# Kernel optimization log

Measured on AMD Instinct MI355X. Metric: run time of the kernel, lower is better.

The kernel has to match this reference:

```python
import jax, jax.numpy as jnp
import numpy as np
from jax import lax

B, C_IN, C_OUT, H, W, K, PAD = 4, 64, 64, 96, 96, 3, 1
K2 = K * K


def setup_inputs() -> dict:
    key = jax.random.key(0)
    k1, k2, k3, k4, k5 = jax.random.split(key, 5)
    x = jax.random.normal(k1, (B, C_IN, H, W), jnp.float32)
    offset = jax.random.normal(k2, (B, 2 * K2, H, W), jnp.float32)
    weight = jax.random.normal(k3, (C_OUT, C_IN, K, K), jnp.float32) * 0.05
    mask_weight = jax.random.normal(k4, (K2, C_IN, K, K), jnp.float32) * 0.05
    mask_bias = jax.random.normal(k5, (K2,), jnp.float32) * 0.05
    return {"x": x, "offset": offset, "weight": weight,
            "mask_weight": mask_weight, "mask_bias": mask_bias}


def _deform_conv2d(x, offset, weight, mask):
    # torchvision ordering: per kernel tap k, offset[:, 2k] is dy, offset[:, 2k+1] is dx
    off_y = offset[:, 0::2]  # [B, K2, H, W]
    off_x = offset[:, 1::2]
    ky, kx = jnp.meshgrid(jnp.arange(K), jnp.arange(K), indexing="ij")
    ky = ky.reshape(K2).astype(x.dtype)
    kx = kx.reshape(K2).astype(x.dtype)
    hh = jnp.arange(H, dtype=x.dtype)
    ww = jnp.arange(W, dtype=x.dtype)
    base_y = hh[None, :, None] - PAD + ky[:, None, None]   # [K2, H, 1]
    base_x = ww[None, None, :] - PAD + kx[:, None, None]   # [K2, 1, W]
    py = base_y[None] + off_y                               # [B, K2, H, W]
    px = base_x[None] + off_x

    y0 = jnp.floor(py)
    x0 = jnp.floor(px)
    wy = py - y0   # bilinear weights
    wx = px - x0
    y0i = y0.astype(jnp.int32)
    x0i = x0.astype(jnp.int32)

    x_flat = x.reshape(B, C_IN, H * W)

    def gather(yy, xx):
        valid = (yy >= 0) & (yy < H) & (xx >= 0) & (xx < W)
        idx = jnp.clip(yy, 0, H - 1) * W + jnp.clip(xx, 0, W - 1)  # [B,K2,H,W]
        idx_f = idx.reshape(B, -1)
        v = jax.vmap(lambda xf, i: xf[:, i])(x_flat, idx_f)  # [B, C, K2*H*W]
        v = v.reshape(B, C_IN, K2, H, W)
        return v * valid[:, None].astype(v.dtype)

    v00 = gather(y0i, x0i)
    v01 = gather(y0i, x0i + 1)
    v10 = gather(y0i + 1, x0i)
    v11 = gather(y0i + 1, x0i + 1)

    wy_ = wy[:, None]  # [B,1,K2,H,W]
    wx_ = wx[:, None]
    sampled = (v00 * (1 - wy_) * (1 - wx_) + v01 * (1 - wy_) * wx_
               + v10 * wy_ * (1 - wx_) + v11 * wy_ * wx_)
    sampled = sampled * mask[:, None]  # modulate by sigmoid mask

    w2 = weight.reshape(C_OUT, C_IN, K2)
    return jnp.einsum("bckhw,ock->bohw", sampled, w2)


def reference(x, offset, weight, mask_weight, mask_bias):
    mask_logits = lax.conv_general_dilated(
        x, mask_weight, window_strides=(1, 1), padding=[(PAD, PAD), (PAD, PAD)],
        dimension_numbers=("NCHW", "OIHW", "NCHW"))
    mask = jax.nn.sigmoid(mask_logits + mask_bias[None, :, None, None])
    return _deform_conv2d(x, offset, weight, mask)
```

## Files before the change

kernel.cpp:

```cpp
#include <hip/hip_runtime.h>
#include <math.h>

#define BB 4
#define CI 64
#define CO 64
#define HH 96
#define WW 96
#define HW (HH*WW)
#define K2 9
#define PADC 1

#define TW 8
#define TH 4
#define TPXT (TW*TH)
#define TBX (WW/TW)
#define TBY (HH/TH)
#define NTILB (TBX*TBY)
#define NTILES (BB*NTILB)

#define WR (TH+9)
#define WC 20
#define SREC 72
#define NSLOT (WR*WC)

typedef __attribute__((ext_vector_type(8))) short short8;
typedef __attribute__((ext_vector_type(4))) float float4v;

#define WF_USHORTS (18*64*32)
#define MWF_USHORTS (18*16*32)

__device__ __forceinline__ float bf2f(short s) {
    return __uint_as_float(((unsigned int)(unsigned short)s) << 16);
}
__device__ __forceinline__ short f2bf(float f) {
    unsigned int u = __float_as_uint(f);
    u = (u + 0x7fffu + ((u >> 16) & 1u)) >> 16;
    return (short)u;
}

__device__ __forceinline__ void unswz(int bid, int* b, int* ty, int* tx) {
    int g = bid & 7, r = bid >> 3;
    *b = g & 3;
    int tile = (g >> 2) * 144 + r;
    *ty = tile / TBX; *tx = tile % TBX;
}

__global__ __launch_bounds__(256) void pack_kernel(const float* __restrict__ wgt,
                                                   const float* __restrict__ mw,
                                                   unsigned short* __restrict__ Wf,
                                                   unsigned short* __restrict__ MWf) {
    int i = blockIdx.x * 256 + threadIdx.x;
    if (i < WF_USHORTS) {
        int frag = i >> 11;
        int o = (i >> 5) & 63;
        int tt = i & 31;
        int k = frag >> 1, cc = frag & 1;
        int c = cc * 32 + tt;
        Wf[i] = (unsigned short)f2bf(wgt[o * 576 + c * 9 + k]);
    } else if (i < WF_USHORTS + MWF_USHORTS) {
        int e = i - WF_USHORTS;
        int frag = e >> 9;
        int m = (e >> 5) & 15;
        int tt = e & 31;
        int q = frag >> 1, cc = frag & 1;
        int c = cc * 32 + tt;
        MWf[e] = (m < 9) ? (unsigned short)f2bf(mw[m * 576 + c * 9 + q]) : 0;
    }
}

__global__ __launch_bounds__(256, 3) void fused_kernel(const float* __restrict__ x,
                                                       const float* __restrict__ off,
                                                       const float* __restrict__ mbias,
                                                       const unsigned short* __restrict__ Wf,
                                                       const unsigned short* __restrict__ MWf,
                                                       float* __restrict__ out) {
    __shared__ __align__(16) unsigned short win[NSLOT * SREC];
    __shared__ float s_mred[2][K2][TPXT];
    __shared__ int   s_idx[K2][4][TPXT];
    __shared__ float s_w[K2][4][TPXT];
    float* part = (float*)win;

    int t = threadIdx.x;
    int lane = t & 63, wv = t >> 6;
    int pg = wv >> 1, ch = wv & 1;
    int n = lane & 15, quad = lane >> 4;
    int b, ty, tx; unswz(blockIdx.x, &b, &ty, &tx);
    int h0 = ty * TH, w0 = tx * TW;
    int wr0 = h0 - 4, wc0 = w0 - 4;
    const float* xb = x + (size_t)b * CI * HW;

    for (int e = t; e < WR * 32 * 5; e += 256) {
        int r = e / 160, rem = e % 160, chp = rem / 5, c4 = rem % 5;
        int row = min(max(wr0 + r, 0), HH - 1);
        int c0c = wc0 + c4 * 4;
        const float* s0 = xb + (size_t)(2 * chp) * HW + row * WW;
        const float* s1 = s0 + HW;
        float v0[4], v1[4];
        if (c0c >= 0 && c0c + 3 < WW) {
            float4v a = *(const float4v*)(s0 + c0c);
            float4v bq = *(const float4v*)(s1 + c0c);
            v0[0]=a[0]; v0[1]=a[1]; v0[2]=a[2]; v0[3]=a[3];
            v1[0]=bq[0]; v1[1]=bq[1]; v1[2]=bq[2]; v1[3]=bq[3];
        } else {
            #pragma unroll
            for (int j = 0; j < 4; j++) {
                int cc2 = min(max(c0c + j, 0), WW - 1);
                v0[j] = s0[cc2]; v1[j] = s1[cc2];
            }
        }
        #pragma unroll
        for (int j = 0; j < 4; j++) {
            unsigned int pk = (unsigned short)f2bf(v0[j]) |
                              ((unsigned int)(unsigned short)f2bf(v1[j]) << 16);
            *(unsigned int*)&win[(r * WC + c4 * 4 + j) * SREC + 2 * chp] = pk;
        }
    }
    __syncthreads();

    int pxl = pg * 16 + n;
    int ly = pxl >> 3, lx = pxl & 7;
    int h = h0 + ly, wcc = w0 + lx;
    int cbase_us = ch * 32 + quad * 8;

    {
        float4v macc = {0.f, 0.f, 0.f, 0.f};
        #pragma unroll
        for (int q = 0; q < 9; q++) {
            int hh = h + q / 3 - 1, ww2 = wcc + q % 3 - 1;
            bool valid = (hh >= 0) && (hh < HH) && (ww2 >= 0) && (ww2 < WW);
            short8 bfrag = {0, 0, 0, 0, 0, 0, 0, 0};
            if (valid) {
                int slot = (hh - wr0) * WC + (ww2 - wc0);
                bfrag = *(const short8*)&win[slot * SREC + cbase_us];
            }
            short8 afrag = *(const short8*)(MWf + ((size_t)((q * 2 + ch) * 16 + n)) * 32 + quad * 8);
            macc = __builtin_amdgcn_mfma_f32_16x16x32_bf16(afrag, bfrag, macc, 0, 0, 0);
        }
        #pragma unroll
        for (int r = 0; r < 4; r++) {
            int row = quad * 4 + r;
            if (row < 9) s_mred[ch][row][pxl] = macc[r];
        }
    }
    __syncthreads();

    for (int e = t; e < K2 * TPXT; e += 256) {
        int k = e >> 5, pe = e & 31;
        int ph = h0 + (pe >> 3), pw = w0 + (pe & 7);
        int p = ph * WW + pw;
        float oy = off[((size_t)b * 2 * K2 + 2 * k) * HW + p];
        float ox = off[((size_t)b * 2 * K2 + 2 * k + 1) * HW + p];
        float s = s_mred[0][k][pe] + s_mred[1][k][pe] + mbias[k];
        float m = 1.f / (1.f + expf(-s));
        float py  = (float)(ph - PADC + k / 3) + oy;
        float pxf = (float)(pw - PADC + k % 3) + ox;
        float y0f = floorf(py), x0f = floorf(pxf);
        float wy = py - y0f, wx = pxf - x0f;
        int y0 = (int)y0f, x0 = (int)x0f;
        int y1 = y0 + 1, x1 = x0 + 1;
        int y0c = min(max(y0, 0), HH - 1), y1c = min(max(y1, 0), HH - 1);
        int x0c = min(max(x0, 0), WW - 1), x1c = min(max(x1, 0), WW - 1);
        bool vy0 = (y0 >= 0) && (y0 < HH), vy1 = (y1 >= 0) && (y1 < HH);
        bool vx0 = (x0 >= 0) && (x0 < WW), vx1 = (x1 >= 0) && (x1 < WW);
        float w00 = (1.f - wy) * (1.f - wx) * m; if (!(vy0 && vx0)) w00 = 0.f;
        float w01 = (1.f - wy) * wx * m;         if (!(vy0 && vx1)) w01 = 0.f;
        float w10 = wy * (1.f - wx) * m;         if (!(vy1 && vx0)) w10 = 0.f;
        float w11 = wy * wx * m;                 if (!(vy1 && vx1)) w11 = 0.f;
        s_idx[k][0][pe] = (y0c << 16) | x0c;
        s_idx[k][1][pe] = (y0c << 16) | x1c;
        s_idx[k][2][pe] = (y1c << 16) | x0c;
        s_idx[k][3][pe] = (y1c << 16) | x1c;
        s_w[k][0][pe] = w00; s_w[k][1][pe] = w01;
        s_w[k][2][pe] = w10; s_w[k][3][pe] = w11;
    }
    __syncthreads();

    float4v acc0 = {0.f, 0.f, 0.f, 0.f};
    float4v acc1 = {0.f, 0.f, 0.f, 0.f};
    float4v acc2 = {0.f, 0.f, 0.f, 0.f};
    float4v acc3 = {0.f, 0.f, 0.f, 0.f};
    const float* xfb = xb + (size_t)(ch * 32 + quad * 8) * HW;

    #pragma unroll
    for (int k = 0; k < 9; k++) {
        short8 U[4];
        #pragma unroll
        for (int cor = 0; cor < 4; cor++) {
            int yx = s_idx[k][cor][pxl];
            int yy = yx >> 16, xx = yx & 0xffff;
            int r = yy - wr0, c = xx - wc0;
            bool inw = ((unsigned)r < (unsigned)WR) && ((unsigned)c < (unsigned)WC);
            short8 u;
            if (inw) {
                u = *(const short8*)&win[(r * WC + c) * SREC + cbase_us];
            } else {
                const float* fs = xfb + yy * WW + xx;
                #pragma unroll
                for (int j = 0; j < 8; j++) u[j] = f2bf(fs[(size_t)j * HW]);
            }
            U[cor] = u;
        }
        float w0 = s_w[k][0][pxl], w1 = s_w[k][1][pxl];
        float w2 = s_w[k][2][pxl], w3 = s_w[k][3][pxl];
        short8 bfrag;
        #pragma unroll
        for (int j = 0; j < 8; j++) {
            float v = bf2f(U[0][j]) * w0 + bf2f(U[1][j]) * w1 +
                      bf2f(U[2][j]) * w2 + bf2f(U[3][j]) * w3;
            bfrag[j] = f2bf(v);
        }
        const unsigned short* wp = Wf + (size_t)((k * 2 + ch) * 64) * 32 + quad * 8;
        short8 a0 = *(const short8*)(wp + (0 * 16 + n) * 32);
        short8 a1 = *(const short8*)(wp + (1 * 16 + n) * 32);
        short8 a2 = *(const short8*)(wp + (2 * 16 + n) * 32);
        short8 a3 = *(const short8*)(wp + (3 * 16 + n) * 32);
        acc0 = __builtin_amdgcn_mfma_f32_16x16x32_bf16(a0, bfrag, acc0, 0, 0, 0);
        acc1 = __builtin_amdgcn_mfma_f32_16x16x32_bf16(a1, bfrag, acc1, 0, 0, 0);
        acc2 = __builtin_amdgcn_mfma_f32_16x16x32_bf16(a2, bfrag, acc2, 0, 0, 0);
        acc3 = __builtin_amdgcn_mfma_f32_16x16x32_bf16(a3, bfrag, acc3, 0, 0, 0);
    }

    __syncthreads();
    if (ch == 1) {
        #pragma unroll
        for (int r = 0; r < 4; r++) {
            part[(pg * 16 + 0 * 4 + r) * 64 + lane] = acc0[r];
            part[(pg * 16 + 1 * 4 + r) * 64 + lane] = acc1[r];
            part[(pg * 16 + 2 * 4 + r) * 64 + lane] = acc2[r];
            part[(pg * 16 + 3 * 4 + r) * 64 + lane] = acc3[r];
        }
    }
    __syncthreads();
    if (ch == 0) {
        float* ob = out + (size_t)b * CO * HW + h * WW + wcc;
        #pragma unroll
        for (int r = 0; r < 4; r++) {
            ob[(size_t)(0 * 16 + quad * 4 + r) * HW] =
                acc0[r] + part[(pg * 16 + 0 * 4 + r) * 64 + lane];
            ob[(size_t)(1 * 16 + quad * 4 + r) * HW] =
                acc1[r] + part[(pg * 16 + 1 * 4 + r) * 64 + lane];
            ob[(size_t)(2 * 16 + quad * 4 + r) * HW] =
                acc2[r] + part[(pg * 16 + 2 * 4 + r) * 64 + lane];
            ob[(size_t)(3 * 16 + quad * 4 + r) * HW] =
                acc3[r] + part[(pg * 16 + 3 * 4 + r) * 64 + lane];
        }
    }
}

extern "C" void kernel_launch(void* const* d_in, const int* in_sizes, int n_in,
                              void* d_out, int out_size, void* d_ws, size_t ws_size,
                              hipStream_t stream) {
    const float* x   = (const float*)d_in[0];
    const float* off = (const float*)d_in[1];
    const float* wgt = (const float*)d_in[2];
    const float* mw  = (const float*)d_in[3];
    const float* mb  = (const float*)d_in[4];
    float* out = (float*)d_out;

    unsigned short* Wf  = (unsigned short*)d_ws;
    unsigned short* MWf = Wf + WF_USHORTS;

    hipLaunchKernelGGL(pack_kernel, dim3((WF_USHORTS + MWF_USHORTS + 255) / 256), dim3(256),
                       0, stream, wgt, mw, Wf, MWf);
    hipLaunchKernelGGL(fused_kernel, dim3(NTILES), dim3(256), 0, stream,
                       x, off, mb, Wf, MWf, out);
}
```

Measured before the change: 101.2 us.

## Precompute LDS byte offsets per corner, vectorize tag loads, use packed bf16 math

The setup phase now stores each bilinear corner as a precomputed LDS byte offset, or a flagged global index, in a pixel-major layout. The gather loop can then fetch all four tags and weights with single 16-byte loads. A wave-uniform fast path skips the per-corner window checks when every lane hits the window. Interpolation uses packed float2 math with hardware v_cvt_pk_bf16_f32 conversion, replacing the manual rounding that was also used in the window fill. The hardware conversion may round NaN or edge cases differently from the old software rounding.

After: 98.61 us. 2.6% less time.

```diff
diff --git a/kernel.cpp b/kernel.cpp
--- a/kernel.cpp
+++ b/kernel.cpp
@@ -25,6 +25,9 @@
 
 typedef __attribute__((ext_vector_type(8))) short short8;
 typedef __attribute__((ext_vector_type(4))) float float4v;
+typedef __attribute__((ext_vector_type(2))) float float2v;
+typedef __attribute__((ext_vector_type(4))) unsigned int uint4v;
+typedef __attribute__((ext_vector_type(4))) int int4v;
 
 #define WF_USHORTS (18*64*32)
 #define MWF_USHORTS (18*16*32)
@@ -36,6 +39,17 @@
     unsigned int u = __float_as_uint(f);
     u = (u + 0x7fffu + ((u >> 16) & 1u)) >> 16;
     return (short)u;
+}
+__device__ __forceinline__ unsigned int cvt_pk_bf16(float lo, float hi) {
+    unsigned int r;
+    asm("v_cvt_pk_bf16_f32 %0, %1, %2" : "=v"(r) : "v"(lo), "v"(hi));
+    return r;
+}
+__device__ __forceinline__ float2v bfpair(unsigned int u) {
+    float2v r;
+    r.x = __uint_as_float(u << 16);
+    r.y = __uint_as_float(u & 0xffff0000u);
+    return r;
 }
 
 __device__ __forceinline__ void unswz(int bid, int* b, int* ty, int* tx) {
@@ -76,8 +90,8 @@
                                                        float* __restrict__ out) {
     __shared__ __align__(16) unsigned short win[NSLOT * SREC];
     __shared__ float s_mred[2][K2][TPXT];
-    __shared__ int   s_idx[K2][4][TPXT];
-    __shared__ float s_w[K2][4][TPXT];
+    __shared__ __align__(16) int   s_tag[K2][TPXT][4];
+    __shared__ __align__(16) float s_wt[K2][TPXT][4];
     float* part = (float*)win;
 
     int t = threadIdx.x;
@@ -110,9 +124,8 @@
         }
         #pragma unroll
         for (int j = 0; j < 4; j++) {
-            unsigned int pk = (unsigned short)f2bf(v0[j]) |
-                              ((unsigned int)(unsigned short)f2bf(v1[j]) << 16);
-            *(unsigned int*)&win[(r * WC + c4 * 4 + j) * SREC + 2 * chp] = pk;
+            *(unsigned int*)&win[(r * WC + c4 * 4 + j) * SREC + 2 * chp] =
+                cvt_pk_bf16(v0[j], v1[j]);
         }
     }
     __syncthreads();
@@ -166,12 +179,21 @@
         float w01 = (1.f - wy) * wx * m;         if (!(vy0 && vx1)) w01 = 0.f;
         float w10 = wy * (1.f - wx) * m;         if (!(vy1 && vx0)) w10 = 0.f;
         float w11 = wy * wx * m;                 if (!(vy1 && vx1)) w11 = 0.f;
-        s_idx[k][0][pe] = (y0c << 16) | x0c;
-        s_idx[k][1][pe] = (y0c << 16) | x1c;
-        s_idx[k][2][pe] = (y1c << 16) | x0c;
-        s_idx[k][3][pe] = (y1c << 16) | x1c;
-        s_w[k][0][pe] = w00; s_w[k][1][pe] = w01;
-        s_w[k][2][pe] = w10; s_w[k][3][pe] = w11;
+        int rA = y0c - wr0, rB = y1c - wr0;
+        int cA = x0c - wc0, cB = x1c - wc0;
+        bool irA = (unsigned)rA < (unsigned)WR, irB = (unsigned)rB < (unsigned)WR;
+        bool jcA = (unsigned)cA < (unsigned)WC, jcB = (unsigned)cB < (unsigned)WC;
+        int gy0 = y0c * WW, gy1 = y1c * WW;
+        s_tag[k][pe][0] = (irA && jcA) ? (rA * WC + cA) * (SREC * 2)
+                                       : (int)(0x80000000u | (unsigned)(gy0 + x0c));
+        s_tag[k][pe][1] = (irA && jcB) ? (rA * WC + cB) * (SREC * 2)
+                                       : (int)(0x80000000u | (unsigned)(gy0 + x1c));
+        s_tag[k][pe][2] = (irB && jcA) ? (rB * WC + cA) * (SREC * 2)
+                                       : (int)(0x80000000u | (unsigned)(gy1 + x0c));
+        s_tag[k][pe][3] = (irB && jcB) ? (rB * WC + cB) * (SREC * 2)
+                                       : (int)(0x80000000u | (unsigned)(gy1 + x1c));
+        s_wt[k][pe][0] = w00; s_wt[k][pe][1] = w01;
+        s_wt[k][pe][2] = w10; s_wt[k][pe][3] = w11;
     }
     __syncthreads();
 
@@ -180,35 +202,48 @@
     float4v acc2 = {0.f, 0.f, 0.f, 0.f};
     float4v acc3 = {0.f, 0.f, 0.f, 0.f};
     const float* xfb = xb + (size_t)(ch * 32 + quad * 8) * HW;
+    const char* wbase = (const char*)win + (size_t)(cbase_us * 2);
 
     #pragma unroll
     for (int k = 0; k < 9; k++) {
-        short8 U[4];
-        #pragma unroll
-        for (int cor = 0; cor < 4; cor++) {
-            int yx = s_idx[k][cor][pxl];
-            int yy = yx >> 16, xx = yx & 0xffff;
-            int r = yy - wr0, c = xx - wc0;
-            bool inw = ((unsigned)r < (unsigned)WR) && ((unsigned)c < (unsigned)WC);
-            short8 u;
-            if (inw) {
-                u = *(const short8*)&win[(r * WC + c) * SREC + cbase_us];
-            } else {
-                const float* fs = xfb + yy * WW + xx;
-                #pragma unroll
-                for (int j = 0; j < 8; j++) u[j] = f2bf(fs[(size_t)j * HW]);
+        int4v tg = *(const int4v*)&s_tag[k][pxl][0];
+        float4v wt = *(const float4v*)&s_wt[k][pxl][0];
+        uint4v Cg[4];
+        if (!__any((tg[0] | tg[1] | tg[2] | tg[3]) < 0)) {
+            #pragma unroll
+            for (int cor = 0; cor < 4; cor++)
+                Cg[cor] = *(const uint4v*)(wbase + tg[cor]);
+        } else {
+            #pragma unroll
+            for (int cor = 0; cor < 4; cor++) {
+                int tag = tg[cor];
+                uint4v u;
+                if (tag >= 0) {
+                    u = *(const uint4v*)(wbase + tag);
+                } else {
+                    const float* fs = xfb + (tag & 0x7fffffff);
+                    #pragma unroll
+                    for (int p2 = 0; p2 < 4; p2++) {
+                        u[p2] = (unsigned int)(unsigned short)f2bf(fs[(size_t)(2 * p2) * HW]) |
+                                ((unsigned int)(unsigned short)f2bf(fs[(size_t)(2 * p2 + 1) * HW]) << 16);
+                    }
+                }
+                Cg[cor] = u;
             }
-            U[cor] = u;
-        }
-        float w0 = s_w[k][0][pxl], w1 = s_w[k][1][pxl];
-        float w2 = s_w[k][2][pxl], w3 = s_w[k][3][pxl];
-        short8 bfrag;
-        #pragma unroll
-        for (int j = 0; j < 8; j++) {
-            float v = bf2f(U[0][j]) * w0 + bf2f(U[1][j]) * w1 +
-                      bf2f(U[2][j]) * w2 + bf2f(U[3][j]) * w3;
-            bfrag[j] = f2bf(v);
-        }
+        }
+        float2v w0v = {wt[0], wt[0]}, w1v = {wt[1], wt[1]};
+        float2v w2v = {wt[2], wt[2]}, w3v = {wt[3], wt[3]};
+        uint4v bfw;
+        #pragma unroll
+        for (int p2 = 0; p2 < 4; p2++) {
+            float2v v = bfpair(Cg[0][p2]) * w0v;
+            v += bfpair(Cg[1][p2]) * w1v;
+            v += bfpair(Cg[2][p2]) * w2v;
+            v += bfpair(Cg[3][p2]) * w3v;
+            bfw[p2] = cvt_pk_bf16(v.x, v.y);
+        }
+        union { uint4v u; short8 s; } cv; cv.u = bfw;
+        short8 bfrag = cv.s;
         const unsigned short* wp = Wf + (size_t)((k * 2 + ch) * 64) * 32 + quad * 8;
         short8 a0 = *(const short8*)(wp + (0 * 16 + n) * 32);
         short8 a1 = *(const short8*)(wp + (1 * 16 + n) * 32);
```
